# Kernel optimization log

Measured on AMD Instinct MI355X. Metric: run time of the kernel, lower is better.

The kernel has to match this reference:

```python
import jax, jax.numpy as jnp
import numpy as np
from math import sqrt

EMBED = 768
HEADS = 12
EPS = 1e-12  # torch F.normalize eps


def setup_inputs() -> dict:
    key = jax.random.key(0)
    ks = jax.random.split(key, 9)
    B, N, E = 8, 4096, EMBED
    s = 1.0 / np.sqrt(E)
    x = jax.random.normal(ks[0], (B, N, E), dtype=jnp.float32)
    Wq = jax.random.normal(ks[1], (E, E), dtype=jnp.float32) * s
    bq = jnp.zeros((E,), dtype=jnp.float32)
    Wk = jax.random.normal(ks[2], (E, E), dtype=jnp.float32) * s
    bk = jnp.zeros((E,), dtype=jnp.float32)
    Wv = jax.random.normal(ks[3], (E, E), dtype=jnp.float32) * s
    bv = jnp.zeros((E,), dtype=jnp.float32)
    Wo = jax.random.normal(ks[4], (E, E), dtype=jnp.float32) * s
    bo = jnp.zeros((E,), dtype=jnp.float32)
    return {"x": x, "Wq": Wq, "bq": bq, "Wk": Wk, "bk": bk,
            "Wv": Wv, "bv": bv, "Wo": Wo, "bo": bo}


def _l2norm_tokens(t):
    # F.normalize(p=2, dim=1): normalize over the token (n) axis
    nrm = jnp.sqrt(jnp.sum(t * t, axis=1, keepdims=True))
    return t / jnp.maximum(nrm, EPS)


def reference(x, Wq, bq, Wk, bk, Wv, bv, Wo, bo):
    B, N, E = x.shape
    h = HEADS
    e = E // h
    q = (x @ Wq + bq).reshape(B, N, h, e)
    k = (x @ Wk + bk).reshape(B, N, h, e)
    v = (x @ Wv + bv).reshape(B, N, h, e)
    q = _l2norm_tokens(q)
    k = _l2norm_tokens(k)
    # cross-covariance attention over channel dim: [b, e, h, e]
    energy = jnp.einsum('bnhe,bnhq->behq', q, k)
    attn = jax.nn.softmax(energy, axis=-1) / sqrt(E)
    out = jnp.einsum('behq,bnhe->bnhq', attn, v)  # [b, n, h, e]
    out = out.reshape(B, N, E)
    return out @ Wo + bo
```

## Files before the change

kernel.cpp:

```cpp
#include <hip/hip_runtime.h>
#include <hip/hip_bf16.h>

typedef short bf16x8 __attribute__((ext_vector_type(8)));
typedef unsigned short u16x8 __attribute__((ext_vector_type(8)));
typedef float f32x4 __attribute__((ext_vector_type(4)));
using bf16 = __hip_bfloat16;

#define EMB 768
#define NHEAD 12
#define BATCH 8
#define NTOK 4096
#define BNTOK 32768

__device__ __forceinline__ float b2f(unsigned short u) {
    union { unsigned int i; float f; } x; x.i = ((unsigned int)u) << 16; return x.f;
}
__device__ __forceinline__ unsigned short f2bu(float f) {
    bf16 h = __float2bfloat16(f);
    return *reinterpret_cast<unsigned short*>(&h);
}

__device__ __forceinline__ void gload_lds16(const void* g, void* l) {
    __builtin_amdgcn_global_load_lds(
        (const __attribute__((address_space(1))) unsigned int*)g,
        (__attribute__((address_space(3))) unsigned int*)l,
        16, 0, 0);
}

__global__ __launch_bounds__(256) void cast_x_kernel(const float* __restrict__ x,
                                                     bf16* __restrict__ xb, int n8) {
    int i = blockIdx.x * blockDim.x + threadIdx.x;
    if (i >= n8) return;
    const float4* xv = (const float4*)x;
    float4 a = xv[i * 2], b = xv[i * 2 + 1];
    u16x8 o;
    o[0] = f2bu(a.x); o[1] = f2bu(a.y); o[2] = f2bu(a.z); o[3] = f2bu(a.w);
    o[4] = f2bu(b.x); o[5] = f2bu(b.y); o[6] = f2bu(b.z); o[7] = f2bu(b.w);
    ((u16x8*)xb)[i] = o;
}

__global__ __launch_bounds__(256) void prep_w_kernel(
    const float* __restrict__ Wq, const float* __restrict__ Wk,
    const float* __restrict__ Wv, const float* __restrict__ Wo,
    const float* __restrict__ bq, const float* __restrict__ bk, const float* __restrict__ bv,
    bf16* __restrict__ WqkvT, bf16* __restrict__ WoT, float* __restrict__ bqkv) {
    const int NQKV = 2304 * 768, NO = 768 * 768;
    int i = blockIdx.x * blockDim.x + threadIdx.x;
    if (i < NQKV) {
        int nrow = i / 768, k = i % 768;
        const float* W = (nrow < 768) ? Wq : (nrow < 1536 ? Wk : Wv);
        int c = nrow % 768;
        WqkvT[i] = __float2bfloat16(W[k * 768 + c]);
    } else if (i < NQKV + NO) {
        int j = i - NQKV; int nrow = j / 768, k = j % 768;
        WoT[j] = __float2bfloat16(Wo[k * 768 + nrow]);
    } else if (i < NQKV + NO + 2304) {
        int j = i - NQKV - NO;
        bqkv[j] = (j < 768) ? bq[j] : (j < 1536 ? bk[j - 768] : bv[j - 1536]);
    }
}

template <int MODE>
__global__ __launch_bounds__(512, 2) void gemm256(
    const bf16* __restrict__ A, const bf16* __restrict__ BT,
    bf16* __restrict__ Q, bf16* __restrict__ Kb, bf16* __restrict__ V,
    const float* __restrict__ bias,
    float* __restrict__ Cout, const float* __restrict__ bo) {
    __shared__ char lds[131072];
    const int NKT = 12;
    const int tid = threadIdx.x;
    const int lane = tid & 63, wid = tid >> 6;
    const int wm = wid >> 2, wn = wid & 3;
    const int lrow = lane & 15, lk = lane >> 4;
    const int xsl = lrow & 3;
    const int lrsw = lrow ^ ((lrow >> 2) & 1);
    const int slotb = (lk ^ xsl) << 4;

    int nwg = gridDim.x * gridDim.y;
    int bid = blockIdx.y * gridDim.x + blockIdx.x;
    int swz = (bid & 7) * (nwg >> 3) + (bid >> 3);
    int bx = swz % gridDim.x, by = swz / gridDim.x;
    const int m0 = by * 256, n0 = bx * 256;

    const int rstg = tid >> 2;
    const int rl = rstg ^ ((rstg >> 2) & 1);
    const int sl8 = (((tid & 3) ^ (rl & 3)) << 3);

    f32x4 acc[8][4] = {};

#define STAGE(tbuf, isb, skh, sktv) do {                                          \
    int skt_ = (sktv); if (skt_ >= NKT) skt_ = NKT - 1;                           \
    const bf16* gp_ = ((isb) ? BT + (size_t)(n0 + rl) * 768                       \
                             : A  + (size_t)(m0 + rl) * 768)                      \
                      + skt_ * 64 + (skh) * 32 + sl8;                             \
    char* lp_ = lds + (tbuf) * 65536 + (isb) * 32768 + (skh) * 16384 + wid * 1024;\
    gload_lds16(gp_, lp_);                                                        \
    gload_lds16(gp_ + (size_t)128 * 768, lp_ + 8192);                             \
} while (0)

#define COMPUTE(cbuf, KH, CM) do {                                                \
    const char* ab_ = lds + (cbuf) * 65536 + (KH) * 16384;                        \
    const char* bb_ = ab_ + 32768;                                                \
    bf16x8 af_[4], bfv_[4];                                                       \
    _Pragma("unroll") for (int mi = 0; mi < 4; ++mi) {                            \
        int pr_ = wm * 128 + (CM) * 64 + mi * 16 + lrsw;                          \
        af_[mi] = *(const bf16x8*)(ab_ + pr_ * 64 + slotb); }                     \
    _Pragma("unroll") for (int ni = 0; ni < 4; ++ni) {                            \
        int pr_ = wn * 64 + ni * 16 + lrsw;                                       \
        bfv_[ni] = *(const bf16x8*)(bb_ + pr_ * 64 + slotb); }                    \
    __builtin_amdgcn_s_setprio(1);                                                \
    _Pragma("unroll") for (int mi = 0; mi < 4; ++mi)                              \
    _Pragma("unroll") for (int ni = 0; ni < 4; ++ni)                              \
        acc[(CM) * 4 + mi][ni] = __builtin_amdgcn_mfma_f32_16x16x32_bf16(         \
            af_[mi], bfv_[ni], acc[(CM) * 4 + mi][ni], 0, 0, 0);                  \
    __builtin_amdgcn_s_setprio(0);                                                \
} while (0)

#define VMC8 asm volatile("s_waitcnt vmcnt(8)" ::: "memory")
#define BAR  __builtin_amdgcn_s_barrier()

    STAGE(0, 0, 0, 0);
    STAGE(0, 1, 0, 0);
    STAGE(0, 0, 1, 0);
    STAGE(0, 1, 1, 0);
    STAGE(1, 0, 0, 1);
    STAGE(1, 1, 0, 1);
    VMC8; BAR;

    for (int i = 0; i < NKT; ++i) {
        const int cb = i & 1, nb = cb ^ 1;
        STAGE(nb, 0, 1, i + 1); COMPUTE(cb, 0, 0); BAR;
        STAGE(nb, 1, 1, i + 1); COMPUTE(cb, 0, 1); VMC8; BAR;
        STAGE(cb, 0, 0, i + 2); COMPUTE(cb, 1, 0); BAR;
        STAGE(cb, 1, 0, i + 2); COMPUTE(cb, 1, 1); VMC8; BAR;
    }

#undef STAGE
#undef COMPUTE
#undef VMC8
#undef BAR

    const int lq = lk;
    if (MODE == 0) {
        const int which = n0 / 768;
        bf16* O = (which == 0) ? Q : (which == 1 ? Kb : V);
        const int cbase = n0 - which * 768 + wn * 64;
#pragma unroll
        for (int ri = 0; ri < 8; ++ri)
#pragma unroll
            for (int ni = 0; ni < 4; ++ni) {
                int gcol = n0 + wn * 64 + ni * 16 + lrow;
                float bia = bias[gcol];
                int col = cbase + ni * 16 + lrow;
                size_t r0 = (size_t)(m0 + wm * 128 + ri * 16 + lq * 4);
#pragma unroll
                for (int r = 0; r < 4; ++r)
                    O[(r0 + r) * 768 + col] = __float2bfloat16(acc[ri][ni][r] + bia);
            }
    } else {
#pragma unroll
        for (int ri = 0; ri < 8; ++ri)
#pragma unroll
            for (int ni = 0; ni < 4; ++ni) {
                int col = n0 + wn * 64 + ni * 16 + lrow;
                float bia = bo[col];
                size_t r0 = (size_t)(m0 + wm * 128 + ri * 16 + lq * 4);
#pragma unroll
                for (int r = 0; r < 4; ++r)
                    Cout[(r0 + r) * 768 + col] = acc[ri][ni][r] + bia;
            }
    }
}

__global__ __launch_bounds__(256) void sumsq_kernel(
    const bf16* __restrict__ Qb, const bf16* __restrict__ Kb,
    float* __restrict__ ssq, float* __restrict__ ssk) {
    int rc = blockIdx.x, ct = blockIdx.y, b = blockIdx.z;
    int col = ct * 256 + threadIdx.x;
    size_t base = ((size_t)b * NTOK + rc * 256) * 768 + col;
    float sq = 0.f, sk = 0.f;
    for (int i = 0; i < 256; ++i) {
        float q = b2f(*(const unsigned short*)&Qb[base + (size_t)i * 768]);
        float k = b2f(*(const unsigned short*)&Kb[base + (size_t)i * 768]);
        sq += q * q; sk += k * k;
    }
    atomicAdd(&ssq[b * 768 + col], sq);
    atomicAdd(&ssk[b * 768 + col], sk);
}

__global__ __launch_bounds__(256) void gram_kernel(
    const bf16* __restrict__ Qb, const bf16* __restrict__ Kb, float* __restrict__ G) {
    int bh = blockIdx.x >> 2, ch = blockIdx.x & 3;
    int b = bh / NHEAD, h = bh % NHEAD;
    const int t0 = ch * 1024;
    __shared__ float Qs[32][64];
    __shared__ float Ks[32][64];
    int tid = threadIdx.x;
    int e0 = (tid >> 4) << 2, j0 = (tid & 15) << 2;
    float acc[4][4] = {};
    const size_t base = ((size_t)b * NTOK) * 768 + h * 64;
    int lt = tid >> 3, lc = (tid & 7) << 3;
    for (int it = 0; it < 32; ++it) {
        int tok = t0 + it * 32;
        u16x8 qv = *(const u16x8*)(Qb + base + (size_t)(tok + lt) * 768 + lc);
        u16x8 kv = *(const u16x8*)(Kb + base + (size_t)(tok + lt) * 768 + lc);
        __syncthreads();
#pragma unroll
        for (int j = 0; j < 8; ++j) { Qs[lt][lc + j] = b2f(qv[j]); Ks[lt][lc + j] = b2f(kv[j]); }
        __syncthreads();
#pragma unroll
        for (int t = 0; t < 32; ++t) {
            float4 q4 = *(const float4*)&Qs[t][e0];
            float4 k4 = *(const float4*)&Ks[t][j0];
            float q[4] = {q4.x, q4.y, q4.z, q4.w};
            float k[4] = {k4.x, k4.y, k4.z, k4.w};
#pragma unroll
            for (int ii = 0; ii < 4; ++ii)
#pragma unroll
                for (int jj = 0; jj < 4; ++jj) acc[ii][jj] = fmaf(q[ii], k[jj], acc[ii][jj]);
        }
    }
#pragma unroll
    for (int ii = 0; ii < 4; ++ii)
#pragma unroll
        for (int jj = 0; jj < 4; ++jj)
            atomicAdd(&G[(size_t)bh * 4096 + (e0 + ii) * 64 + (j0 + jj)], acc[ii][jj]);
}

__global__ __launch_bounds__(64) void softmax_kernel(
    const float* __restrict__ G, const float* __restrict__ ssq, const float* __restrict__ ssk,
    bf16* __restrict__ attnT) {
    int bh = blockIdx.x; int b = bh / NHEAD, h = bh % NHEAD;
    int e = threadIdx.x;
    const float* g = G + (size_t)bh * 4096 + e * 64;
    float nq = fmaxf(sqrtf(ssq[b * 768 + h * 64 + e]), 1e-12f);
    float row[64];
    float mx = -1e30f;
#pragma unroll
    for (int j = 0; j < 64; ++j) {
        float nk = fmaxf(sqrtf(ssk[b * 768 + h * 64 + j]), 1e-12f);
        float en = g[j] / (nq * nk);
        row[j] = en;
        mx = fmaxf(mx, en);
    }
    float s = 0.f;
#pragma unroll
    for (int j = 0; j < 64; ++j) { row[j] = __expf(row[j] - mx); s += row[j]; }
    float inv = 0.036084391824351615f / s;
#pragma unroll
    for (int j = 0; j < 64; ++j)
        attnT[(size_t)bh * 4096 + j * 64 + e] = __float2bfloat16(row[j] * inv);
}

__global__ __launch_bounds__(256) void pv_kernel(
    const bf16* __restrict__ V, const bf16* __restrict__ attnT, bf16* __restrict__ Y) {
    int tch = blockIdx.x;
    int h = blockIdx.y, b = blockIdx.z;
    int bh = b * NHEAD + h;
    __shared__ bf16 Ats[64 * 64];
    int tid = threadIdx.x, lane = tid & 63, wid = tid >> 6;
    {
        const u16x8* src = (const u16x8*)(attnT + (size_t)bh * 4096);
        u16x8* dst = (u16x8*)Ats;
        dst[tid] = src[tid];
        dst[tid + 256] = src[tid + 256];
    }
    __syncthreads();
    f32x4 acc[4][4] = {};
    const int lrow = lane & 15, lk = lane >> 4;
    const int trow0 = tch * 256 + wid * 64;
#pragma unroll
    for (int ks = 0; ks < 2; ++ks) {
        bf16x8 a[4], bfr[4];
#pragma unroll
        for (int mi = 0; mi < 4; ++mi)
            a[mi] = *(const bf16x8*)(V + (size_t)(b * NTOK + trow0 + mi * 16 + lrow) * 768 +
                                     h * 64 + ks * 32 + lk * 8);
        const bf16x8* Bv = (const bf16x8*)Ats;
#pragma unroll
        for (int ni = 0; ni < 4; ++ni) bfr[ni] = Bv[(ni * 16 + lrow) * 8 + ks * 4 + lk];
#pragma unroll
        for (int mi = 0; mi < 4; ++mi)
#pragma unroll
            for (int ni = 0; ni < 4; ++ni)
                acc[mi][ni] = __builtin_amdgcn_mfma_f32_16x16x32_bf16(a[mi], bfr[ni], acc[mi][ni], 0, 0, 0);
    }
    const int lq = lane >> 4;
#pragma unroll
    for (int mi = 0; mi < 4; ++mi)
#pragma unroll
        for (int ni = 0; ni < 4; ++ni) {
            int col = ni * 16 + lrow;
#pragma unroll
            for (int r = 0; r < 4; ++r) {
                int row = trow0 + mi * 16 + lq * 4 + r;
                Y[(size_t)(b * NTOK + row) * 768 + h * 64 + col] = __float2bfloat16(acc[mi][ni][r]);
            }
        }
}

extern "C" void kernel_launch(void* const* d_in, const int* in_sizes, int n_in,
                              void* d_out, int out_size, void* d_ws, size_t ws_size,
                              hipStream_t stream) {
    const float* x  = (const float*)d_in[0];
    const float* Wq = (const float*)d_in[1];
    const float* bq = (const float*)d_in[2];
    const float* Wk = (const float*)d_in[3];
    const float* bk = (const float*)d_in[4];
    const float* Wv = (const float*)d_in[5];
    const float* bv = (const float*)d_in[6];
    const float* Wo = (const float*)d_in[7];
    const float* bo = (const float*)d_in[8];
    float* out = (float*)d_out;

    char* ws = (char*)d_ws;
    bf16*  xb    = (bf16*)(ws + 0);
    bf16*  WqkvT = (bf16*)(ws + 50331648);
    bf16*  WoT   = (bf16*)(ws + 53870592);
    float* bqkv  = (float*)(ws + 55050240);
    bf16*  Qb    = (bf16*)(ws + 55059456);
    bf16*  Kb    = (bf16*)(ws + 105391104);
    bf16*  Vb    = (bf16*)(ws + 155722752);
    float* ssq   = (float*)(ws + 206054400);
    float* ssk   = (float*)(ws + 206078976);
    float* G     = (float*)(ws + 206103552);
    bf16*  attnT = (bf16*)(ws + 207676416);
    bf16*  Yb    = xb;

    hipMemsetAsync(ws + 206054400, 0, 24576 + 24576 + 1572864, stream);

    cast_x_kernel<<<12288, 256, 0, stream>>>(x, xb, BNTOK * EMB / 8);
    prep_w_kernel<<<9225, 256, 0, stream>>>(Wq, Wk, Wv, Wo, bq, bk, bv, WqkvT, WoT, bqkv);

    gemm256<0><<<dim3(9, 128), 512, 0, stream>>>(xb, WqkvT, Qb, Kb, Vb, bqkv, nullptr, nullptr);

    sumsq_kernel<<<dim3(16, 3, 8), 256, 0, stream>>>(Qb, Kb, ssq, ssk);
    gram_kernel<<<384, 256, 0, stream>>>(Qb, Kb, G);
    softmax_kernel<<<96, 64, 0, stream>>>(G, ssq, ssk, attnT);
    pv_kernel<<<dim3(16, NHEAD, BATCH), 256, 0, stream>>>(Vb, attnT, Yb);

    gemm256<1><<<dim3(3, 128), 512, 0, stream>>>(Yb, WoT, nullptr, nullptr, nullptr, nullptr, out, bo);
}
```

Baseline: 377.0 us.

## Fold attention into per-batch output weights and use MFMA transposed gram

Instead of computing attn·V per token and then the Wo projection, it folds the per-head attention matrix into a per-batch combined weight (Wo composed with attn), so the final GEMM reads V directly and the pv kernel disappears. The QKV GEMM now writes Q and K transposed (channel-major), so a new MFMA gram kernel computes the Gram matrix and the sum-of-squares norms in one pass, replacing two separate kernels. The GEMM drops its LDS swizzle in favour of a fragment-linear layout, loads the B fragment once per k-half, and changes launch bounds to one block per CU. This trades an extra small weight-folding kernel and per-batch weight reads, plus possible LDS bank conflicts and lower occupancy, for removing a full token pass and a kernel.

```diff
diff --git a/kernel.cpp b/kernel.cpp
--- a/kernel.cpp
+++ b/kernel.cpp
@@ -3,6 +3,7 @@
 
 typedef short bf16x8 __attribute__((ext_vector_type(8)));
 typedef unsigned short u16x8 __attribute__((ext_vector_type(8)));
+typedef unsigned short us4 __attribute__((ext_vector_type(4)));
 typedef float f32x4 __attribute__((ext_vector_type(4)));
 using bf16 = __hip_bfloat16;
 
@@ -61,9 +62,9 @@
 }
 
 template <int MODE>
-__global__ __launch_bounds__(512, 2) void gemm256(
+__global__ __launch_bounds__(512, 1) void gemm256(
     const bf16* __restrict__ A, const bf16* __restrict__ BT,
-    bf16* __restrict__ Q, bf16* __restrict__ Kb, bf16* __restrict__ V,
+    bf16* __restrict__ QT, bf16* __restrict__ KT, bf16* __restrict__ V,
     const float* __restrict__ bias,
     float* __restrict__ Cout, const float* __restrict__ bo) {
     __shared__ char lds[131072];
@@ -72,9 +73,6 @@
     const int lane = tid & 63, wid = tid >> 6;
     const int wm = wid >> 2, wn = wid & 3;
     const int lrow = lane & 15, lk = lane >> 4;
-    const int xsl = lrow & 3;
-    const int lrsw = lrow ^ ((lrow >> 2) & 1);
-    const int slotb = (lk ^ xsl) << 4;
 
     int nwg = gridDim.x * gridDim.y;
     int bid = blockIdx.y * gridDim.x + blockIdx.x;
@@ -82,42 +80,46 @@
     int bx = swz % gridDim.x, by = swz / gridDim.x;
     const int m0 = by * 256, n0 = bx * 256;
 
-    const int rstg = tid >> 2;
-    const int rl = rstg ^ ((rstg >> 2) & 1);
-    const int sl8 = (((tid & 3) ^ (rl & 3)) << 3);
+    const bf16* bt = BT + (MODE == 1 ? (size_t)(m0 >> 12) * 589824 : 0);
+
+    const int srow = wid * 16 + lrow;
+    const int scol = ((lane >> 4) & 3) << 3;
 
     f32x4 acc[8][4] = {};
 
-#define STAGE(tbuf, isb, skh, sktv) do {                                          \
-    int skt_ = (sktv); if (skt_ >= NKT) skt_ = NKT - 1;                           \
-    const bf16* gp_ = ((isb) ? BT + (size_t)(n0 + rl) * 768                       \
-                             : A  + (size_t)(m0 + rl) * 768)                      \
-                      + skt_ * 64 + (skh) * 32 + sl8;                             \
-    char* lp_ = lds + (tbuf) * 65536 + (isb) * 32768 + (skh) * 16384 + wid * 1024;\
-    gload_lds16(gp_, lp_);                                                        \
-    gload_lds16(gp_ + (size_t)128 * 768, lp_ + 8192);                             \
+#define STAGE(tbuf, isb, skh, sktv) do {                                           \
+    int skt_ = (sktv); if (skt_ >= NKT) skt_ = NKT - 1;                            \
+    const bf16* gp_ = ((isb) ? bt + (size_t)(n0 + srow) * 768                      \
+                             : A  + (size_t)(m0 + srow) * 768)                     \
+                      + skt_ * 64 + (skh) * 32 + scol;                             \
+    char* lp_ = lds + (tbuf) * 65536 + (isb) * 32768 + (skh) * 16384 + wid * 1024; \
+    gload_lds16(gp_, lp_);                                                         \
+    gload_lds16(gp_ + (size_t)128 * 768, lp_ + 8192);                              \
 } while (0)
 
-#define COMPUTE(cbuf, KH, CM) do {                                                \
-    const char* ab_ = lds + (cbuf) * 65536 + (KH) * 16384;                        \
-    const char* bb_ = ab_ + 32768;                                                \
-    bf16x8 af_[4], bfv_[4];                                                       \
-    _Pragma("unroll") for (int mi = 0; mi < 4; ++mi) {                            \
-        int pr_ = wm * 128 + (CM) * 64 + mi * 16 + lrsw;                          \
-        af_[mi] = *(const bf16x8*)(ab_ + pr_ * 64 + slotb); }                     \
-    _Pragma("unroll") for (int ni = 0; ni < 4; ++ni) {                            \
-        int pr_ = wn * 64 + ni * 16 + lrsw;                                       \
-        bfv_[ni] = *(const bf16x8*)(bb_ + pr_ * 64 + slotb); }                    \
-    __builtin_amdgcn_s_setprio(1);                                                \
-    _Pragma("unroll") for (int mi = 0; mi < 4; ++mi)                              \
-    _Pragma("unroll") for (int ni = 0; ni < 4; ++ni)                              \
-        acc[(CM) * 4 + mi][ni] = __builtin_amdgcn_mfma_f32_16x16x32_bf16(         \
-            af_[mi], bfv_[ni], acc[(CM) * 4 + mi][ni], 0, 0, 0);                  \
-    __builtin_amdgcn_s_setprio(0);                                                \
+#define LOADB(cbuf, KH) do {                                                       \
+    const char* bb_ = lds + (cbuf) * 65536 + 32768 + (KH) * 16384;                 \
+    _Pragma("unroll") for (int ni = 0; ni < 4; ++ni)                               \
+        bre[ni] = *(const bf16x8*)(bb_ + (wn * 4 + ni) * 1024 + lane * 16);        \
+} while (0)
+
+#define COMPUTE(cbuf, KH, CM) do {                                                 \
+    const char* ab_ = lds + (cbuf) * 65536 + (KH) * 16384;                         \
+    bf16x8 af_[4];                                                                 \
+    _Pragma("unroll") for (int mi = 0; mi < 4; ++mi)                               \
+        af_[mi] = *(const bf16x8*)(ab_ + (wm * 8 + (CM) * 4 + mi) * 1024 + lane * 16); \
+    __builtin_amdgcn_s_setprio(1);                                                 \
+    _Pragma("unroll") for (int mi = 0; mi < 4; ++mi)                               \
+    _Pragma("unroll") for (int ni = 0; ni < 4; ++ni)                               \
+        acc[(CM) * 4 + mi][ni] = __builtin_amdgcn_mfma_f32_16x16x32_bf16(          \
+            af_[mi], bre[ni], acc[(CM) * 4 + mi][ni], 0, 0, 0);                    \
+    __builtin_amdgcn_s_setprio(0);                                                 \
 } while (0)
 
 #define VMC8 asm volatile("s_waitcnt vmcnt(8)" ::: "memory")
 #define BAR  __builtin_amdgcn_s_barrier()
+
+    bf16x8 bre[4];
 
     STAGE(0, 0, 0, 0);
     STAGE(0, 1, 0, 0);
@@ -129,34 +131,53 @@
 
     for (int i = 0; i < NKT; ++i) {
         const int cb = i & 1, nb = cb ^ 1;
-        STAGE(nb, 0, 1, i + 1); COMPUTE(cb, 0, 0); BAR;
+        STAGE(nb, 0, 1, i + 1); LOADB(cb, 0); COMPUTE(cb, 0, 0); BAR;
         STAGE(nb, 1, 1, i + 1); COMPUTE(cb, 0, 1); VMC8; BAR;
-        STAGE(cb, 0, 0, i + 2); COMPUTE(cb, 1, 0); BAR;
+        STAGE(cb, 0, 0, i + 2); LOADB(cb, 1); COMPUTE(cb, 1, 0); BAR;
         STAGE(cb, 1, 0, i + 2); COMPUTE(cb, 1, 1); VMC8; BAR;
     }
 
 #undef STAGE
+#undef LOADB
 #undef COMPUTE
 #undef VMC8
 #undef BAR
 
-    const int lq = lk;
     if (MODE == 0) {
         const int which = n0 / 768;
-        bf16* O = (which == 0) ? Q : (which == 1 ? Kb : V);
-        const int cbase = n0 - which * 768 + wn * 64;
-#pragma unroll
-        for (int ri = 0; ri < 8; ++ri)
-#pragma unroll
-            for (int ni = 0; ni < 4; ++ni) {
-                int gcol = n0 + wn * 64 + ni * 16 + lrow;
-                float bia = bias[gcol];
-                int col = cbase + ni * 16 + lrow;
-                size_t r0 = (size_t)(m0 + wm * 128 + ri * 16 + lq * 4);
-#pragma unroll
-                for (int r = 0; r < 4; ++r)
-                    O[(r0 + r) * 768 + col] = __float2bfloat16(acc[ri][ni][r] + bia);
-            }
+        if (which < 2) {
+            bf16* T = (which == 0) ? QT : KT;
+            const int b = m0 >> 12;
+            const int tb = (m0 & 4095) + wm * 128 + lk * 4;
+#pragma unroll
+            for (int ri = 0; ri < 8; ++ri)
+#pragma unroll
+                for (int ni = 0; ni < 4; ++ni) {
+                    int gcol = n0 + wn * 64 + ni * 16 + lrow;
+                    int chan = gcol - which * 768;
+                    float bia = bias[gcol];
+                    int tokl = tb + ri * 16;
+                    us4 pk;
+                    pk[0] = f2bu(acc[ri][ni][0] + bia);
+                    pk[1] = f2bu(acc[ri][ni][1] + bia);
+                    pk[2] = f2bu(acc[ri][ni][2] + bia);
+                    pk[3] = f2bu(acc[ri][ni][3] + bia);
+                    *(us4*)&T[((size_t)b * 768 + chan) * 4096 + tokl] = pk;
+                }
+        } else {
+#pragma unroll
+            for (int ri = 0; ri < 8; ++ri)
+#pragma unroll
+                for (int ni = 0; ni < 4; ++ni) {
+                    int gcol = n0 + wn * 64 + ni * 16 + lrow;
+                    int chan = gcol - 1536;
+                    float bia = bias[gcol];
+                    size_t r0 = (size_t)(m0 + wm * 128 + ri * 16 + lk * 4);
+#pragma unroll
+                    for (int r = 0; r < 4; ++r)
+                        V[(r0 + r) * 768 + chan] = __float2bfloat16(acc[ri][ni][r] + bia);
+                }
+        }
     } else {
 #pragma unroll
         for (int ri = 0; ri < 8; ++ri)
@@ -164,7 +185,7 @@
             for (int ni = 0; ni < 4; ++ni) {
                 int col = n0 + wn * 64 + ni * 16 + lrow;
                 float bia = bo[col];
-                size_t r0 = (size_t)(m0 + wm * 128 + ri * 16 + lq * 4);
+                size_t r0 = (size_t)(m0 + wm * 128 + ri * 16 + lk * 4);
 #pragma unroll
                 for (int r = 0; r < 4; ++r)
                     Cout[(r0 + r) * 768 + col] = acc[ri][ni][r] + bia;
@@ -172,64 +193,74 @@
     }
 }
 
-__global__ __launch_bounds__(256) void sumsq_kernel(
-    const bf16* __restrict__ Qb, const bf16* __restrict__ Kb,
-    float* __restrict__ ssq, float* __restrict__ ssk) {
-    int rc = blockIdx.x, ct = blockIdx.y, b = blockIdx.z;
-    int col = ct * 256 + threadIdx.x;
-    size_t base = ((size_t)b * NTOK + rc * 256) * 768 + col;
-    float sq = 0.f, sk = 0.f;
-    for (int i = 0; i < 256; ++i) {
-        float q = b2f(*(const unsigned short*)&Qb[base + (size_t)i * 768]);
-        float k = b2f(*(const unsigned short*)&Kb[base + (size_t)i * 768]);
-        sq += q * q; sk += k * k;
-    }
-    atomicAdd(&ssq[b * 768 + col], sq);
-    atomicAdd(&ssk[b * 768 + col], sk);
-}
-
-__global__ __launch_bounds__(256) void gram_kernel(
-    const bf16* __restrict__ Qb, const bf16* __restrict__ Kb, float* __restrict__ G) {
-    int bh = blockIdx.x >> 2, ch = blockIdx.x & 3;
-    int b = bh / NHEAD, h = bh % NHEAD;
-    const int t0 = ch * 1024;
-    __shared__ float Qs[32][64];
-    __shared__ float Ks[32][64];
-    int tid = threadIdx.x;
-    int e0 = (tid >> 4) << 2, j0 = (tid & 15) << 2;
-    float acc[4][4] = {};
-    const size_t base = ((size_t)b * NTOK) * 768 + h * 64;
-    int lt = tid >> 3, lc = (tid & 7) << 3;
-    for (int it = 0; it < 32; ++it) {
-        int tok = t0 + it * 32;
-        u16x8 qv = *(const u16x8*)(Qb + base + (size_t)(tok + lt) * 768 + lc);
-        u16x8 kv = *(const u16x8*)(Kb + base + (size_t)(tok + lt) * 768 + lc);
-        __syncthreads();
-#pragma unroll
-        for (int j = 0; j < 8; ++j) { Qs[lt][lc + j] = b2f(qv[j]); Ks[lt][lc + j] = b2f(kv[j]); }
-        __syncthreads();
-#pragma unroll
-        for (int t = 0; t < 32; ++t) {
-            float4 q4 = *(const float4*)&Qs[t][e0];
-            float4 k4 = *(const float4*)&Ks[t][j0];
-            float q[4] = {q4.x, q4.y, q4.z, q4.w};
-            float k[4] = {k4.x, k4.y, k4.z, k4.w};
-#pragma unroll
-            for (int ii = 0; ii < 4; ++ii)
-#pragma unroll
-                for (int jj = 0; jj < 4; ++jj) acc[ii][jj] = fmaf(q[ii], k[jj], acc[ii][jj]);
+__global__ __launch_bounds__(256) void gram_mfma_kernel(
+    const bf16* __restrict__ QT, const bf16* __restrict__ KT,
+    float* __restrict__ G, float* __restrict__ ssq, float* __restrict__ ssk) {
+    const int kc = blockIdx.x, bh = blockIdx.y;
+    const int b = bh / NHEAD, h = bh % NHEAD;
+    const int tid = threadIdx.x, lane = tid & 63, w = tid >> 6;
+    const int lrow = lane & 15, lk = lane >> 4;
+    const int t0 = kc * 512 + w * 128;
+
+    f32x4 acc[4][4] = {};
+    float sqp[4] = {}, skp[4] = {};
+    const size_t qbase = ((size_t)b * 768 + h * 64) * 4096;
+
+#pragma unroll
+    for (int kk = 0; kk < 4; ++kk) {
+        bf16x8 a[4], bb[4];
+#pragma unroll
+        for (int mi = 0; mi < 4; ++mi)
+            a[mi] = *(const bf16x8*)(QT + qbase + (size_t)(mi * 16 + lrow) * 4096 +
+                                     t0 + kk * 32 + lk * 8);
+#pragma unroll
+        for (int ni = 0; ni < 4; ++ni)
+            bb[ni] = *(const bf16x8*)(KT + qbase + (size_t)(ni * 16 + lrow) * 4096 +
+                                      t0 + kk * 32 + lk * 8);
+#pragma unroll
+        for (int mi = 0; mi < 4; ++mi) {
+#pragma unroll
+            for (int j = 0; j < 8; ++j) {
+                float qv = b2f((unsigned short)a[mi][j]);
+                float kv = b2f((unsigned short)bb[mi][j]);
+                sqp[mi] = fmaf(qv, qv, sqp[mi]);
+                skp[mi] = fmaf(kv, kv, skp[mi]);
+            }
         }
-    }
-#pragma unroll
-    for (int ii = 0; ii < 4; ++ii)
-#pragma unroll
-        for (int jj = 0; jj < 4; ++jj)
-            atomicAdd(&G[(size_t)bh * 4096 + (e0 + ii) * 64 + (j0 + jj)], acc[ii][jj]);
+#pragma unroll
+        for (int mi = 0; mi < 4; ++mi)
+#pragma unroll
+            for (int ni = 0; ni < 4; ++ni)
+                acc[mi][ni] = __builtin_amdgcn_mfma_f32_16x16x32_bf16(a[mi], bb[ni], acc[mi][ni], 0, 0, 0);
+    }
+
+#pragma unroll
+    for (int mi = 0; mi < 4; ++mi) {
+        float vq = sqp[mi], vk = skp[mi];
+        vq += __shfl_down(vq, 32); vq += __shfl_down(vq, 16);
+        vk += __shfl_down(vk, 32); vk += __shfl_down(vk, 16);
+        if (lane < 16) {
+            atomicAdd(&ssq[b * 768 + h * 64 + mi * 16 + lrow], vq);
+            atomicAdd(&ssk[b * 768 + h * 64 + mi * 16 + lrow], vk);
+        }
+    }
+
+    float* g = G + (size_t)bh * 4096;
+#pragma unroll
+    for (int mi = 0; mi < 4; ++mi)
+#pragma unroll
+        for (int ni = 0; ni < 4; ++ni)
+#pragma unroll
+            for (int r = 0; r < 4; ++r) {
+                int e = mi * 16 + lk * 4 + r;
+                int j = ni * 16 + lrow;
+                atomicAdd(&g[e * 64 + j], acc[mi][ni][r]);
+            }
 }
 
 __global__ __launch_bounds__(64) void softmax_kernel(
     const float* __restrict__ G, const float* __restrict__ ssq, const float* __restrict__ ssk,
-    bf16* __restrict__ attnT) {
+    bf16* __restrict__ attnA) {
     int bh = blockIdx.x; int b = bh / NHEAD, h = bh % NHEAD;
     int e = threadIdx.x;
     const float* g = G + (size_t)bh * 4096 + e * 64;
@@ -249,54 +280,46 @@
     float inv = 0.036084391824351615f / s;
 #pragma unroll
     for (int j = 0; j < 64; ++j)
-        attnT[(size_t)bh * 4096 + j * 64 + e] = __float2bfloat16(row[j] * inv);
-}
-
-__global__ __launch_bounds__(256) void pv_kernel(
-    const bf16* __restrict__ V, const bf16* __restrict__ attnT, bf16* __restrict__ Y) {
-    int tch = blockIdx.x;
-    int h = blockIdx.y, b = blockIdx.z;
-    int bh = b * NHEAD + h;
-    __shared__ bf16 Ats[64 * 64];
-    int tid = threadIdx.x, lane = tid & 63, wid = tid >> 6;
-    {
-        const u16x8* src = (const u16x8*)(attnT + (size_t)bh * 4096);
-        u16x8* dst = (u16x8*)Ats;
-        dst[tid] = src[tid];
-        dst[tid + 256] = src[tid + 256];
-    }
-    __syncthreads();
-    f32x4 acc[4][4] = {};
+        attnA[(size_t)bh * 4096 + e * 64 + j] = __float2bfloat16(row[j] * inv);
+}
+
+__global__ __launch_bounds__(256) void wtilde_kernel(
+    const bf16* __restrict__ WoT, const bf16* __restrict__ attnA,
+    bf16* __restrict__ WtT) {
+    const int ns = blockIdx.x, bh = blockIdx.y;
+    const int b = bh / NHEAD, h = bh % NHEAD;
+    const int tid = threadIdx.x, lane = tid & 63, w = tid >> 6;
     const int lrow = lane & 15, lk = lane >> 4;
-    const int trow0 = tch * 256 + wid * 64;
-#pragma unroll
-    for (int ks = 0; ks < 2; ++ks) {
-        bf16x8 a[4], bfr[4];
-#pragma unroll
-        for (int mi = 0; mi < 4; ++mi)
-            a[mi] = *(const bf16x8*)(V + (size_t)(b * NTOK + trow0 + mi * 16 + lrow) * 768 +
-                                     h * 64 + ks * 32 + lk * 8);
-        const bf16x8* Bv = (const bf16x8*)Ats;
-#pragma unroll
-        for (int ni = 0; ni < 4; ++ni) bfr[ni] = Bv[(ni * 16 + lrow) * 8 + ks * 4 + lk];
-#pragma unroll
-        for (int mi = 0; mi < 4; ++mi)
+    const int nbase = ns * 192 + w * 48;
+
+    f32x4 acc[3][4] = {};
+#pragma unroll
+    for (int kk = 0; kk < 2; ++kk) {
+        bf16x8 a[3], bb[4];
+#pragma unroll
+        for (int mi = 0; mi < 3; ++mi)
+            a[mi] = *(const bf16x8*)(WoT + (size_t)(nbase + mi * 16 + lrow) * 768 +
+                                     h * 64 + kk * 32 + lk * 8);
+#pragma unroll
+        for (int ni = 0; ni < 4; ++ni)
+            bb[ni] = *(const bf16x8*)(attnA + (size_t)bh * 4096 +
+                                      (ni * 16 + lrow) * 64 + kk * 32 + lk * 8);
+#pragma unroll
+        for (int mi = 0; mi < 3; ++mi)
 #pragma unroll
             for (int ni = 0; ni < 4; ++ni)
-                acc[mi][ni] = __builtin_amdgcn_mfma_f32_16x16x32_bf16(a[mi], bfr[ni], acc[mi][ni], 0, 0, 0);
-    }
-    const int lq = lane >> 4;
-#pragma unroll
-    for (int mi = 0; mi < 4; ++mi)
-#pragma unroll
-        for (int ni = 0; ni < 4; ++ni) {
-            int col = ni * 16 + lrow;
+                acc[mi][ni] = __builtin_amdgcn_mfma_f32_16x16x32_bf16(a[mi], bb[ni], acc[mi][ni], 0, 0, 0);
+    }
+#pragma unroll
+    for (int mi = 0; mi < 3; ++mi)
+#pragma unroll
+        for (int ni = 0; ni < 4; ++ni)
 #pragma unroll
             for (int r = 0; r < 4; ++r) {
-                int row = trow0 + mi * 16 + lq * 4 + r;
-                Y[(size_t)(b * NTOK + row) * 768 + h * 64 + col] = __float2bfloat16(acc[mi][ni][r]);
+                int n = nbase + mi * 16 + lk * 4 + r;
+                int e = ni * 16 + lrow;
+                WtT[((size_t)b * 768 + n) * 768 + h * 64 + e] = __float2bfloat16(acc[mi][ni][r]);
             }
-        }
 }
 
 extern "C" void kernel_launch(void* const* d_in, const int* in_sizes, int n_in,
@@ -318,26 +341,25 @@
     bf16*  WqkvT = (bf16*)(ws + 50331648);
     bf16*  WoT   = (bf16*)(ws + 53870592);
     float* bqkv  = (float*)(ws + 55050240);
-    bf16*  Qb    = (bf16*)(ws + 55059456);
-    bf16*  Kb    = (bf16*)(ws + 105391104);
+    bf16*  QT    = (bf16*)(ws + 55059456);
+    bf16*  KT    = (bf16*)(ws + 105391104);
     bf16*  Vb    = (bf16*)(ws + 155722752);
     float* ssq   = (float*)(ws + 206054400);
     float* ssk   = (float*)(ws + 206078976);
     float* G     = (float*)(ws + 206103552);
-    bf16*  attnT = (bf16*)(ws + 207676416);
-    bf16*  Yb    = xb;
+    bf16*  attnA = (bf16*)(ws + 207676416);
+    bf16*  WtT   = xb;
 
     hipMemsetAsync(ws + 206054400, 0, 24576 + 24576 + 1572864, stream);
 
     cast_x_kernel<<<12288, 256, 0, stream>>>(x, xb, BNTOK * EMB / 8);
     prep_w_kernel<<<9225, 256, 0, stream>>>(Wq, Wk, Wv, Wo, bq, bk, bv, WqkvT, WoT, bqkv);
 
-    gemm256<0><<<dim3(9, 128), 512, 0, stream>>>(xb, WqkvT, Qb, Kb, Vb, bqkv, nullptr, nullptr);
-
-    sumsq_kernel<<<dim3(16, 3, 8), 256, 0, stream>>>(Qb, Kb, ssq, ssk);
-    gram_kernel<<<384, 256, 0, stream>>>(Qb, Kb, G);
-    softmax_kernel<<<96, 64, 0, stream>>>(G, ssq, ssk, attnT);
-    pv_kernel<<<dim3(16, NHEAD, BATCH), 256, 0, stream>>>(Vb, attnT, Yb);
-
-    gemm256<1><<<dim3(3, 128), 512, 0, stream>>>(Yb, WoT, nullptr, nullptr, nullptr, nullptr, out, bo);
-}
+    gemm256<0><<<dim3(9, 128), 512, 0, stream>>>(xb, WqkvT, QT, KT, Vb, bqkv, nullptr, nullptr);
+
+    gram_mfma_kernel<<<dim3(8, 96), 256, 0, stream>>>(QT, KT, G, ssq, ssk);
+    softmax_kernel<<<96, 64, 0, stream>>>(G, ssq, ssk, attnA);
+    wtilde_kernel<<<dim3(4, 96), 256, 0, stream>>>(WoT, attnA, WtT);
+
+    gemm256<1><<<dim3(3, 128), 512, 0, stream>>>(Vb, WtT, nullptr, nullptr, nullptr, nullptr, out, bo);
+}
```

New measurement: 357.2 us. 5.3% less time.
